# Optimization experiments

Measured on AMD Instinct MI355X. Metric: run time of the kernel, lower is better.

Reference implementation:

```python
import jax, jax.numpy as jnp
import numpy as np

TAGSET = 64
START = 0
END = 63
NEG = -10000.0


def setup_inputs() -> dict:
    key = jax.random.key(0)
    k1, k2, k3 = jax.random.split(key, 3)
    B, T, K = 256, 1024, TAGSET
    feats = jax.random.normal(k1, (B, T, K), dtype=jnp.float32)
    tags = jax.random.randint(k2, (B, T), 0, K, dtype=jnp.int64)
    masks = jnp.ones((B, T), dtype=jnp.float32)
    transitions = jax.random.normal(k3, (K, K), dtype=jnp.float32)
    transitions = transitions.at[START, :].set(NEG)
    transitions = transitions.at[:, END].set(NEG)
    return {"feats": feats, "transitions": transitions, "tags": tags, "masks": masks}


def _forward_alg(feats, transitions, masks):
    # feats: [B,T,K], masks: [B,T], transitions: [K,K]
    B, T, K = feats.shape
    alpha0 = jnp.full((B, K), NEG, dtype=feats.dtype).at[:, START].set(0.0)

    def step(alpha, xs):
        f_t, m_t = xs  # [B,K], [B]
        # transitions[i,j] + alpha[b,j], logsumexp over previous tag j
        scores = transitions[None, :, :] + alpha[:, None, :]  # [B,K,K]
        new = jax.nn.logsumexp(scores, axis=-1) + f_t  # [B,K]
        m = m_t[:, None]
        alpha = new * m + alpha * (1.0 - m)
        return alpha, None

    feats_t = jnp.swapaxes(feats[:, 1:], 0, 1)  # [T-1,B,K]
    masks_t = jnp.swapaxes(masks[:, 1:], 0, 1)  # [T-1,B]
    alpha, _ = jax.lax.scan(step, alpha0, (feats_t, masks_t))
    return jax.nn.logsumexp(alpha, axis=-1)  # [B]


def _score_sentence(feats, transitions, tags, masks):
    # transitions[tags_t, tags_{t-1}] + feats[t, tags_t], masked, summed over t>=1
    trans_score = transitions[tags[:, 1:], tags[:, :-1]]  # [B,T-1]
    emit_score = jnp.take_along_axis(feats[:, 1:], tags[:, 1:, None], axis=-1)[..., 0]
    return ((trans_score + emit_score) * masks[:, 1:]).sum(axis=-1)  # [B]


def reference(feats, transitions, tags, masks):
    forward_score = _forward_alg(feats, transitions, masks)
    gold_score = _score_sentence(feats, transitions, tags, masks)
    return jnp.mean(forward_score - gold_score)
```

## Files before the change

### kernel.cpp

```cpp
#include <hip/hip_runtime.h>

#define KK 64
#define TT 1024
#define BB 256
#define START_TAG 0

typedef float v2f __attribute__((ext_vector_type(2)));
typedef float v4f __attribute__((ext_vector_type(4)));

__device__ __forceinline__ float lane_bcast(float v, int lane) {
    return __int_as_float(__builtin_amdgcn_readlane(__float_as_int(v), lane));
}

#define PKMUL(D, S, E) asm("v_pk_mul_f32 %0, %1, %2"     : "=v"(D) : "v"(S), "v"(E));
#define PKFMA(D, S, E) asm("v_pk_fma_f32 %0, %1, %2, %0" : "+v"(D) : "v"(S), "v"(E));
#define PKADD(D, X, Y) asm("v_pk_add_f32 %0, %1, %2"     : "=v"(D) : "v"(X), "v"(Y));

#define DECLP(k) v2f et##k = { __expf(trow[2*(k)]), __expf(trow[2*(k)+1]) };
#define PINP(p,q,r,s) asm volatile("" : "+v"(et##p), "+v"(et##q), "+v"(et##r), "+v"(et##s));

#define DO_STEP(EFV, MKV, RN) { \
    abuf[i] = a; \
    const v4f* rb_ = reinterpret_cast<const v4f*>(abuf); \
    v4f w0 = rb_[0],  w1 = rb_[1],  w2 = rb_[2],  w3 = rb_[3]; \
    v4f w4 = rb_[4],  w5 = rb_[5],  w6 = rb_[6],  w7 = rb_[7]; \
    v4f w8 = rb_[8],  w9 = rb_[9],  w10 = rb_[10], w11 = rb_[11]; \
    v4f w12 = rb_[12], w13 = rb_[13], w14 = rb_[14], w15 = rb_[15]; \
    v2f acc0, acc1, acc2, acc3; \
    PKMUL(acc0, w0.xy, et0)   PKMUL(acc1, w0.zw, et1) \
    PKMUL(acc2, w1.xy, et2)   PKMUL(acc3, w1.zw, et3) \
    PKFMA(acc0, w2.xy, et4)   PKFMA(acc1, w2.zw, et5) \
    PKFMA(acc2, w3.xy, et6)   PKFMA(acc3, w3.zw, et7) \
    PKFMA(acc0, w4.xy, et8)   PKFMA(acc1, w4.zw, et9) \
    PKFMA(acc2, w5.xy, et10)  PKFMA(acc3, w5.zw, et11) \
    PKFMA(acc0, w6.xy, et12)  PKFMA(acc1, w6.zw, et13) \
    PKFMA(acc2, w7.xy, et14)  PKFMA(acc3, w7.zw, et15) \
    PKFMA(acc0, w8.xy, et16)  PKFMA(acc1, w8.zw, et17) \
    PKFMA(acc2, w9.xy, et18)  PKFMA(acc3, w9.zw, et19) \
    PKFMA(acc0, w10.xy, et20) PKFMA(acc1, w10.zw, et21) \
    PKFMA(acc2, w11.xy, et22) PKFMA(acc3, w11.zw, et23) \
    PKFMA(acc0, w12.xy, et24) PKFMA(acc1, w12.zw, et25) \
    PKFMA(acc2, w13.xy, et26) PKFMA(acc3, w13.zw, et27) \
    PKFMA(acc0, w14.xy, et28) PKFMA(acc1, w14.zw, et29) \
    PKFMA(acc2, w15.xy, et30) PKFMA(acc3, w15.zw, et31) \
    v2f accA, accB, accC; \
    PKADD(accA, acc0, acc1) \
    PKADD(accB, acc2, acc3) \
    PKADD(accC, accA, accB) \
    float s_ = accC.x + accC.y; \
    float anew = s_ * (EFV); \
    a = ((MKV) != 0.0f) ? anew : a; \
    if (RN) { \
        float a1 = fmaxf(lane_bcast(a, 1), 1e-37f); \
        a *= __builtin_amdgcn_rcpf(a1); \
        offset += __logf(a1); \
    } \
}

__global__ __launch_bounds__(64)
__attribute__((amdgpu_waves_per_eu(1, 1)))
void crf_forward_kernel(
    const float* __restrict__ feats,
    const float* __restrict__ trans,
    const float* __restrict__ masks,
    const int*   __restrict__ tags,
    float* __restrict__ out)
{
    const int b = blockIdx.x;
    const int i = threadIdx.x;

    __shared__ __align__(16) float abuf[KK];

    const float* trow = trans + i * KK;
    DECLP(0)  DECLP(1)  DECLP(2)  DECLP(3)  DECLP(4)  DECLP(5)  DECLP(6)  DECLP(7)
    DECLP(8)  DECLP(9)  DECLP(10) DECLP(11) DECLP(12) DECLP(13) DECLP(14) DECLP(15)
    DECLP(16) DECLP(17) DECLP(18) DECLP(19) DECLP(20) DECLP(21) DECLP(22) DECLP(23)
    DECLP(24) DECLP(25) DECLP(26) DECLP(27) DECLP(28) DECLP(29) DECLP(30) DECLP(31)
    PINP(0,1,2,3)     PINP(4,5,6,7)     PINP(8,9,10,11)   PINP(12,13,14,15)
    PINP(16,17,18,19) PINP(20,21,22,23) PINP(24,25,26,27) PINP(28,29,30,31)

    float a = (i == START_TAG) ? 1.0f : 0.0f;
    float offset = 0.0f;

    const float* fb = feats + (size_t)b * TT * KK;
    const float* mb = masks + (size_t)b * TT;

    float cf0 = fb[1 * KK + i], cf1 = fb[2 * KK + i];
    float cf2 = fb[3 * KK + i], cf3 = fb[4 * KK + i];
    float cm0 = mb[1], cm1 = mb[2], cm2 = mb[3], cm3 = mb[4];

    for (int t0 = 1; t0 < TT; t0 += 4) {
        int p0 = (t0 + 4 < TT) ? t0 + 4 : TT - 1;
        int p1 = (t0 + 5 < TT) ? t0 + 5 : TT - 1;
        int p2 = (t0 + 6 < TT) ? t0 + 6 : TT - 1;
        int p3 = (t0 + 7 < TT) ? t0 + 7 : TT - 1;
        float nf0 = fb[p0 * KK + i], nf1 = fb[p1 * KK + i];
        float nf2 = fb[p2 * KK + i], nf3 = fb[p3 * KK + i];
        float nm0 = mb[p0], nm1 = mb[p1], nm2 = mb[p2], nm3 = mb[p3];

        float ef0 = __expf(cf0), ef1 = __expf(cf1);
        float ef2 = __expf(cf2), ef3 = __expf(cf3);

        DO_STEP(ef0, cm0, 0)
        DO_STEP(ef1, cm1, 0)
        DO_STEP(ef2, cm2, 0)
        float m3 = (t0 + 3 < TT) ? cm3 : 0.0f;
        DO_STEP(ef3, m3, 1)

        cf0 = nf0; cf1 = nf1; cf2 = nf2; cf3 = nf3;
        cm0 = nm0; cm1 = nm1; cm2 = nm2; cm3 = nm3;
    }

    float s = a;
    #pragma unroll
    for (int off = 32; off >= 1; off >>= 1)
        s += __shfl_xor(s, off, 64);
    float fwd_score = offset + __logf(s);

    const int* tg = tags + b * TT;
    float g = 0.f;
    for (int t = 1 + i; t < TT; t += 64) {
        int ct = tg[t], pt = tg[t - 1];
        g += (trans[ct * KK + pt] + fb[t * KK + ct]) * mb[t];
    }
    #pragma unroll
    for (int off = 32; off >= 1; off >>= 1)
        g += __shfl_xor(g, off, 64);

    if (i == 0) atomicAdd(out, (fwd_score - g) * (1.0f / (float)BB));
}

extern "C" void kernel_launch(void* const* d_in, const int* in_sizes, int n_in,
                              void* d_out, int out_size, void* d_ws, size_t ws_size,
                              hipStream_t stream) {
    const float* feats = (const float*)d_in[0];
    const float* trans = (const float*)d_in[1];
    const int*   tags  = (const int*)d_in[2];
    const float* masks = (const float*)d_in[3];
    float* out = (float*)d_out;

    hipMemsetAsync(out, 0, sizeof(float), stream);
    crf_forward_kernel<<<BB, 64, 0, stream>>>(feats, trans, masks, tags, out);
}
```

Before: 297.8 us.

## Compute own-row block of alpha dot product via DPP row_ror instead of LDS

Splits each step's 64-term matrix-vector product into two parts. The 16 terms from the lane's own DPP row come from cross-lane row_ror DPP multiply/FMA on the live alpha register. The other 48 terms still come from LDS reads of the other three rows. This cuts LDS read volume per step by a quarter and overlaps DPP arithmetic with LDS latency. In exchange it adds hand-written DPP asm, s_nop hazard padding, and permuted transition exponent tables, which adds latency on the serial recurrence.

```diff
diff --git a/kernel.cpp b/kernel.cpp
--- a/kernel.cpp
+++ b/kernel.cpp
@@ -16,38 +16,49 @@
 #define PKFMA(D, S, E) asm("v_pk_fma_f32 %0, %1, %2, %0" : "+v"(D) : "v"(S), "v"(E));
 #define PKADD(D, X, Y) asm("v_pk_add_f32 %0, %1, %2"     : "=v"(D) : "v"(X), "v"(Y));
 
-#define DECLP(k) v2f et##k = { __expf(trow[2*(k)]), __expf(trow[2*(k)+1]) };
-#define PINP(p,q,r,s) asm volatile("" : "+v"(et##p), "+v"(et##q), "+v"(et##r), "+v"(et##s));
+#define RORMOVI(D, K) \
+    asm("v_mov_b32 %0, %1 row_ror:" #K " row_mask:0xf bank_mask:0xf" \
+        : "=v"(D) : "v"(lid));
+#define RORMUL(D, K, E) \
+    asm("v_mul_f32 %0, %1, %2 row_ror:" #K " row_mask:0xf bank_mask:0xf" \
+        : "=v"(D) : "v"(a), "v"(E));
+#define RORFMA(D, K, E) \
+    asm("v_fmac_f32 %0, %1, %2 row_ror:" #K " row_mask:0xf bank_mask:0xf" \
+        : "+v"(D) : "v"(a), "v"(E));
 
 #define DO_STEP(EFV, MKV, RN) { \
     abuf[i] = a; \
-    const v4f* rb_ = reinterpret_cast<const v4f*>(abuf); \
-    v4f w0 = rb_[0],  w1 = rb_[1],  w2 = rb_[2],  w3 = rb_[3]; \
-    v4f w4 = rb_[4],  w5 = rb_[5],  w6 = rb_[6],  w7 = rb_[7]; \
-    v4f w8 = rb_[8],  w9 = rb_[9],  w10 = rb_[10], w11 = rb_[11]; \
-    v4f w12 = rb_[12], w13 = rb_[13], w14 = rb_[14], w15 = rb_[15]; \
-    v2f acc0, acc1, acc2, acc3; \
-    PKMUL(acc0, w0.xy, et0)   PKMUL(acc1, w0.zw, et1) \
-    PKMUL(acc2, w1.xy, et2)   PKMUL(acc3, w1.zw, et3) \
-    PKFMA(acc0, w2.xy, et4)   PKFMA(acc1, w2.zw, et5) \
-    PKFMA(acc2, w3.xy, et6)   PKFMA(acc3, w3.zw, et7) \
-    PKFMA(acc0, w4.xy, et8)   PKFMA(acc1, w4.zw, et9) \
-    PKFMA(acc2, w5.xy, et10)  PKFMA(acc3, w5.zw, et11) \
-    PKFMA(acc0, w6.xy, et12)  PKFMA(acc1, w6.zw, et13) \
-    PKFMA(acc2, w7.xy, et14)  PKFMA(acc3, w7.zw, et15) \
-    PKFMA(acc0, w8.xy, et16)  PKFMA(acc1, w8.zw, et17) \
-    PKFMA(acc2, w9.xy, et18)  PKFMA(acc3, w9.zw, et19) \
-    PKFMA(acc0, w10.xy, et20) PKFMA(acc1, w10.zw, et21) \
-    PKFMA(acc2, w11.xy, et22) PKFMA(acc3, w11.zw, et23) \
-    PKFMA(acc0, w12.xy, et24) PKFMA(acc1, w12.zw, et25) \
-    PKFMA(acc2, w13.xy, et26) PKFMA(acc3, w13.zw, et27) \
-    PKFMA(acc0, w14.xy, et28) PKFMA(acc1, w14.zw, et29) \
-    PKFMA(acc2, w15.xy, et30) PKFMA(acc3, w15.zw, et31) \
-    v2f accA, accB, accC; \
-    PKADD(accA, acc0, acc1) \
-    PKADD(accB, acc2, acc3) \
-    PKADD(accC, accA, accB) \
-    float s_ = accC.x + accC.y; \
+    const v4f* pA_ = reinterpret_cast<const v4f*>(abuf + cb1); \
+    const v4f* pB_ = reinterpret_cast<const v4f*>(abuf + cb2); \
+    const v4f* pC_ = reinterpret_cast<const v4f*>(abuf + cb3); \
+    v4f wA0 = pA_[0], wA1 = pA_[1], wA2 = pA_[2], wA3 = pA_[3]; \
+    v4f wB0 = pB_[0], wB1 = pB_[1], wB2 = pB_[2], wB3 = pB_[3]; \
+    v4f wC0 = pC_[0], wC1 = pC_[1], wC2 = pC_[2], wC3 = pC_[3]; \
+    float sA = a * er0; \
+    float sB; RORMUL(sB, 1, er1) \
+    RORFMA(sA, 2,  er2)  RORFMA(sB, 3,  er3) \
+    RORFMA(sA, 4,  er4)  RORFMA(sB, 5,  er5) \
+    RORFMA(sA, 6,  er6)  RORFMA(sB, 7,  er7) \
+    RORFMA(sA, 8,  er8)  RORFMA(sB, 9,  er9) \
+    RORFMA(sA, 10, er10) RORFMA(sB, 11, er11) \
+    RORFMA(sA, 12, er12) RORFMA(sB, 13, er13) \
+    RORFMA(sA, 14, er14) RORFMA(sB, 15, er15) \
+    v2f q0, q1, q2, q3; \
+    PKMUL(q0, wA0.xy, eA0) PKMUL(q1, wA0.zw, eA1) \
+    PKMUL(q2, wA1.xy, eA2) PKMUL(q3, wA1.zw, eA3) \
+    PKFMA(q0, wA2.xy, eA4) PKFMA(q1, wA2.zw, eA5) \
+    PKFMA(q2, wA3.xy, eA6) PKFMA(q3, wA3.zw, eA7) \
+    PKFMA(q0, wB0.xy, eB0) PKFMA(q1, wB0.zw, eB1) \
+    PKFMA(q2, wB1.xy, eB2) PKFMA(q3, wB1.zw, eB3) \
+    PKFMA(q0, wB2.xy, eB4) PKFMA(q1, wB2.zw, eB5) \
+    PKFMA(q2, wB3.xy, eB6) PKFMA(q3, wB3.zw, eB7) \
+    PKFMA(q0, wC0.xy, eC0) PKFMA(q1, wC0.zw, eC1) \
+    PKFMA(q2, wC1.xy, eC2) PKFMA(q3, wC1.zw, eC3) \
+    PKFMA(q0, wC2.xy, eC4) PKFMA(q1, wC2.zw, eC5) \
+    PKFMA(q2, wC3.xy, eC6) PKFMA(q3, wC3.zw, eC7) \
+    v2f qA, qB, qC; \
+    PKADD(qA, q0, q1) PKADD(qB, q2, q3) PKADD(qC, qA, qB) \
+    float s_ = (qC.x + qC.y) + (sA + sB); \
     float anew = s_ * (EFV); \
     a = ((MKV) != 0.0f) ? anew : a; \
     if (RN) { \
@@ -55,7 +66,10 @@
         a *= __builtin_amdgcn_rcpf(a1); \
         offset += __logf(a1); \
     } \
+    asm volatile("s_nop 1" : "+v"(a));  \
 }
+
+#define PIN4(p,q,r,s) asm volatile("" : "+v"(p), "+v"(q), "+v"(r), "+v"(s));
 
 __global__ __launch_bounds__(64)
 __attribute__((amdgpu_waves_per_eu(1, 1)))
@@ -68,19 +82,50 @@
 {
     const int b = blockIdx.x;
     const int i = threadIdx.x;
+    const int r = (i >> 4) & 3;
+    const int rowbase = i & 48;
 
     __shared__ __align__(16) float abuf[KK];
 
     const float* trow = trans + i * KK;
-    DECLP(0)  DECLP(1)  DECLP(2)  DECLP(3)  DECLP(4)  DECLP(5)  DECLP(6)  DECLP(7)
-    DECLP(8)  DECLP(9)  DECLP(10) DECLP(11) DECLP(12) DECLP(13) DECLP(14) DECLP(15)
-    DECLP(16) DECLP(17) DECLP(18) DECLP(19) DECLP(20) DECLP(21) DECLP(22) DECLP(23)
-    DECLP(24) DECLP(25) DECLP(26) DECLP(27) DECLP(28) DECLP(29) DECLP(30) DECLP(31)
-    PINP(0,1,2,3)     PINP(4,5,6,7)     PINP(8,9,10,11)   PINP(12,13,14,15)
-    PINP(16,17,18,19) PINP(20,21,22,23) PINP(24,25,26,27) PINP(28,29,30,31)
+
+    int lid = i & 15;
+    asm volatile("s_nop 1" : "+v"(lid));
+    int x1, x2, x3, x4, x5, x6, x7, x8, x9, x10, x11, x12, x13, x14, x15;
+    RORMOVI(x1, 1)   RORMOVI(x2, 2)   RORMOVI(x3, 3)   RORMOVI(x4, 4)
+    RORMOVI(x5, 5)   RORMOVI(x6, 6)   RORMOVI(x7, 7)   RORMOVI(x8, 8)
+    RORMOVI(x9, 9)   RORMOVI(x10, 10) RORMOVI(x11, 11) RORMOVI(x12, 12)
+    RORMOVI(x13, 13) RORMOVI(x14, 14) RORMOVI(x15, 15)
+    float er0  = __expf(trow[rowbase + lid]);
+    float er1  = __expf(trow[rowbase + x1]),  er2  = __expf(trow[rowbase + x2]);
+    float er3  = __expf(trow[rowbase + x3]),  er4  = __expf(trow[rowbase + x4]);
+    float er5  = __expf(trow[rowbase + x5]),  er6  = __expf(trow[rowbase + x6]);
+    float er7  = __expf(trow[rowbase + x7]),  er8  = __expf(trow[rowbase + x8]);
+    float er9  = __expf(trow[rowbase + x9]),  er10 = __expf(trow[rowbase + x10]);
+    float er11 = __expf(trow[rowbase + x11]), er12 = __expf(trow[rowbase + x12]);
+    float er13 = __expf(trow[rowbase + x13]), er14 = __expf(trow[rowbase + x14]);
+    float er15 = __expf(trow[rowbase + x15]);
+
+    const int cb1 = ((r + 1) & 3) << 4;
+    const int cb2 = ((r + 2) & 3) << 4;
+    const int cb3 = ((r + 3) & 3) << 4;
+#define DECLE(nm, cb, p) v2f nm = { __expf(trow[(cb) + 2*(p)]), __expf(trow[(cb) + 2*(p) + 1]) };
+    DECLE(eA0, cb1, 0) DECLE(eA1, cb1, 1) DECLE(eA2, cb1, 2) DECLE(eA3, cb1, 3)
+    DECLE(eA4, cb1, 4) DECLE(eA5, cb1, 5) DECLE(eA6, cb1, 6) DECLE(eA7, cb1, 7)
+    DECLE(eB0, cb2, 0) DECLE(eB1, cb2, 1) DECLE(eB2, cb2, 2) DECLE(eB3, cb2, 3)
+    DECLE(eB4, cb2, 4) DECLE(eB5, cb2, 5) DECLE(eB6, cb2, 6) DECLE(eB7, cb2, 7)
+    DECLE(eC0, cb3, 0) DECLE(eC1, cb3, 1) DECLE(eC2, cb3, 2) DECLE(eC3, cb3, 3)
+    DECLE(eC4, cb3, 4) DECLE(eC5, cb3, 5) DECLE(eC6, cb3, 6) DECLE(eC7, cb3, 7)
+
+    PIN4(er0, er1, er2, er3)   PIN4(er4, er5, er6, er7)
+    PIN4(er8, er9, er10, er11) PIN4(er12, er13, er14, er15)
+    PIN4(eA0, eA1, eA2, eA3)   PIN4(eA4, eA5, eA6, eA7)
+    PIN4(eB0, eB1, eB2, eB3)   PIN4(eB4, eB5, eB6, eB7)
+    PIN4(eC0, eC1, eC2, eC3)   PIN4(eC4, eC5, eC6, eC7)
 
     float a = (i == START_TAG) ? 1.0f : 0.0f;
     float offset = 0.0f;
+    asm volatile("s_nop 1" : "+v"(a));
 
     const float* fb = feats + (size_t)b * TT * KK;
     const float* mb = masks + (size_t)b * TT;
```

Measured after the change: 298.4 us. About the same (+0.2%).

## Replace LDS alpha broadcast with permlane swaps and DPP row-rotate FMAs

Applied to the files above, without the earlier changes.

Each recurrence step no longer writes alpha to shared memory and reads all 64 values back. Instead, permlane32/permlane16 swaps give each lane four alpha values from different rows, and DPP row_ror FMAs sweep the 16 rotations. The exp(transition) table is re-gathered per lane to match that rotation order. This removes the LDS store-to-load latency from the serial chain, but it uses scalar FMAs instead of packed ones and depends on s_nop hazard padding for correctness.

```diff
diff --git a/kernel.cpp b/kernel.cpp
--- a/kernel.cpp
+++ b/kernel.cpp
@@ -5,49 +5,42 @@
 #define BB 256
 #define START_TAG 0
 
-typedef float v2f __attribute__((ext_vector_type(2)));
-typedef float v4f __attribute__((ext_vector_type(4)));
-
 __device__ __forceinline__ float lane_bcast(float v, int lane) {
     return __int_as_float(__builtin_amdgcn_readlane(__float_as_int(v), lane));
 }
 
-#define PKMUL(D, S, E) asm("v_pk_mul_f32 %0, %1, %2"     : "=v"(D) : "v"(S), "v"(E));
-#define PKFMA(D, S, E) asm("v_pk_fma_f32 %0, %1, %2, %0" : "+v"(D) : "v"(S), "v"(E));
-#define PKADD(D, X, Y) asm("v_pk_add_f32 %0, %1, %2"     : "=v"(D) : "v"(X), "v"(Y));
+#define SWAPL32(X, Y) asm("v_permlane32_swap_b32 %0, %1" : "+v"(X), "+v"(Y));
+#define SWAPL16(X, Y) asm("v_permlane16_swap_b32 %0, %1" : "+v"(X), "+v"(Y));
 
-#define DECLP(k) v2f et##k = { __expf(trow[2*(k)]), __expf(trow[2*(k)+1]) };
-#define PINP(p,q,r,s) asm volatile("" : "+v"(et##p), "+v"(et##q), "+v"(et##r), "+v"(et##s));
+#define RMOVI(D, S, K) \
+    asm("v_mov_b32 %0, %1 row_ror:" #K " row_mask:0xf bank_mask:0xf" \
+        : "=v"(D) : "v"(S));
+#define RFMA(D, S, K, E) \
+    asm("v_fmac_f32 %0, %1, %2 row_ror:" #K " row_mask:0xf bank_mask:0xf" \
+        : "+v"(D) : "v"(S), "v"(E));
+
+#define GATHER(dst, src, K) { int x_; RMOVI(x_, src, K) dst = __expf(trow[x_]); }
+
+#define PIN4(p,q,r,s) asm volatile("" : "+v"(p), "+v"(q), "+v"(r), "+v"(s));
+
+#define FMAROW(K) \
+    RFMA(c0, U,  K, etA##K) RFMA(c1, U2, K, etB##K) \
+    RFMA(c2, V,  K, etC##K) RFMA(c3, V2, K, etD##K)
 
 #define DO_STEP(EFV, MKV, RN) { \
-    abuf[i] = a; \
-    const v4f* rb_ = reinterpret_cast<const v4f*>(abuf); \
-    v4f w0 = rb_[0],  w1 = rb_[1],  w2 = rb_[2],  w3 = rb_[3]; \
-    v4f w4 = rb_[4],  w5 = rb_[5],  w6 = rb_[6],  w7 = rb_[7]; \
-    v4f w8 = rb_[8],  w9 = rb_[9],  w10 = rb_[10], w11 = rb_[11]; \
-    v4f w12 = rb_[12], w13 = rb_[13], w14 = rb_[14], w15 = rb_[15]; \
-    v2f acc0, acc1, acc2, acc3; \
-    PKMUL(acc0, w0.xy, et0)   PKMUL(acc1, w0.zw, et1) \
-    PKMUL(acc2, w1.xy, et2)   PKMUL(acc3, w1.zw, et3) \
-    PKFMA(acc0, w2.xy, et4)   PKFMA(acc1, w2.zw, et5) \
-    PKFMA(acc2, w3.xy, et6)   PKFMA(acc3, w3.zw, et7) \
-    PKFMA(acc0, w4.xy, et8)   PKFMA(acc1, w4.zw, et9) \
-    PKFMA(acc2, w5.xy, et10)  PKFMA(acc3, w5.zw, et11) \
-    PKFMA(acc0, w6.xy, et12)  PKFMA(acc1, w6.zw, et13) \
-    PKFMA(acc2, w7.xy, et14)  PKFMA(acc3, w7.zw, et15) \
-    PKFMA(acc0, w8.xy, et16)  PKFMA(acc1, w8.zw, et17) \
-    PKFMA(acc2, w9.xy, et18)  PKFMA(acc3, w9.zw, et19) \
-    PKFMA(acc0, w10.xy, et20) PKFMA(acc1, w10.zw, et21) \
-    PKFMA(acc2, w11.xy, et22) PKFMA(acc3, w11.zw, et23) \
-    PKFMA(acc0, w12.xy, et24) PKFMA(acc1, w12.zw, et25) \
-    PKFMA(acc2, w13.xy, et26) PKFMA(acc3, w13.zw, et27) \
-    PKFMA(acc0, w14.xy, et28) PKFMA(acc1, w14.zw, et29) \
-    PKFMA(acc2, w15.xy, et30) PKFMA(acc3, w15.zw, et31) \
-    v2f accA, accB, accC; \
-    PKADD(accA, acc0, acc1) \
-    PKADD(accB, acc2, acc3) \
-    PKADD(accC, accA, accB) \
-    float s_ = accC.x + accC.y; \
+    float U = a, V = a; \
+    asm volatile("s_nop 1" : "+v"(U), "+v"(V)); \
+    SWAPL32(U, V) \
+    float U2 = U, V2 = V; \
+    asm volatile("s_nop 1" : "+v"(U), "+v"(U2), "+v"(V), "+v"(V2)); \
+    SWAPL16(U, U2) \
+    SWAPL16(V, V2) \
+    asm volatile("s_nop 1" : "+v"(U), "+v"(U2), "+v"(V), "+v"(V2)); \
+    float c0 = U * etA0, c1 = U2 * etB0, c2 = V * etC0, c3 = V2 * etD0; \
+    FMAROW(1)  FMAROW(2)  FMAROW(3)  FMAROW(4)  FMAROW(5) \
+    FMAROW(6)  FMAROW(7)  FMAROW(8)  FMAROW(9)  FMAROW(10) \
+    FMAROW(11) FMAROW(12) FMAROW(13) FMAROW(14) FMAROW(15) \
+    float s_ = (c0 + c1) + (c2 + c3); \
     float anew = s_ * (EFV); \
     a = ((MKV) != 0.0f) ? anew : a; \
     if (RN) { \
@@ -69,15 +62,58 @@
     const int b = blockIdx.x;
     const int i = threadIdx.x;
 
-    __shared__ __align__(16) float abuf[KK];
+    const float* trow = trans + i * KK;
 
-    const float* trow = trans + i * KK;
-    DECLP(0)  DECLP(1)  DECLP(2)  DECLP(3)  DECLP(4)  DECLP(5)  DECLP(6)  DECLP(7)
-    DECLP(8)  DECLP(9)  DECLP(10) DECLP(11) DECLP(12) DECLP(13) DECLP(14) DECLP(15)
-    DECLP(16) DECLP(17) DECLP(18) DECLP(19) DECLP(20) DECLP(21) DECLP(22) DECLP(23)
-    DECLP(24) DECLP(25) DECLP(26) DECLP(27) DECLP(28) DECLP(29) DECLP(30) DECLP(31)
-    PINP(0,1,2,3)     PINP(4,5,6,7)     PINP(8,9,10,11)   PINP(12,13,14,15)
-    PINP(16,17,18,19) PINP(20,21,22,23) PINP(24,25,26,27) PINP(28,29,30,31)
+    int lid = i;
+    asm volatile("s_nop 1" : "+v"(lid));
+    int jU = lid, jV = lid;
+    asm volatile("s_nop 1" : "+v"(jU), "+v"(jV));
+    SWAPL32(jU, jV)
+    int jU2 = jU, jV2 = jV;
+    asm volatile("s_nop 1" : "+v"(jU), "+v"(jU2), "+v"(jV), "+v"(jV2));
+    SWAPL16(jU, jU2)
+    SWAPL16(jV, jV2)
+    asm volatile("s_nop 1" : "+v"(jU), "+v"(jU2), "+v"(jV), "+v"(jV2));
+
+    float etA0, etA1, etA2, etA3, etA4, etA5, etA6, etA7,
+          etA8, etA9, etA10, etA11, etA12, etA13, etA14, etA15;
+    float etB0, etB1, etB2, etB3, etB4, etB5, etB6, etB7,
+          etB8, etB9, etB10, etB11, etB12, etB13, etB14, etB15;
+    float etC0, etC1, etC2, etC3, etC4, etC5, etC6, etC7,
+          etC8, etC9, etC10, etC11, etC12, etC13, etC14, etC15;
+    float etD0, etD1, etD2, etD3, etD4, etD5, etD6, etD7,
+          etD8, etD9, etD10, etD11, etD12, etD13, etD14, etD15;
+    etA0 = __expf(trow[jU]);  etB0 = __expf(trow[jU2]);
+    etC0 = __expf(trow[jV]);  etD0 = __expf(trow[jV2]);
+    GATHER(etA1, jU, 1)   GATHER(etA2, jU, 2)   GATHER(etA3, jU, 3)
+    GATHER(etA4, jU, 4)   GATHER(etA5, jU, 5)   GATHER(etA6, jU, 6)
+    GATHER(etA7, jU, 7)   GATHER(etA8, jU, 8)   GATHER(etA9, jU, 9)
+    GATHER(etA10, jU, 10) GATHER(etA11, jU, 11) GATHER(etA12, jU, 12)
+    GATHER(etA13, jU, 13) GATHER(etA14, jU, 14) GATHER(etA15, jU, 15)
+    GATHER(etB1, jU2, 1)   GATHER(etB2, jU2, 2)   GATHER(etB3, jU2, 3)
+    GATHER(etB4, jU2, 4)   GATHER(etB5, jU2, 5)   GATHER(etB6, jU2, 6)
+    GATHER(etB7, jU2, 7)   GATHER(etB8, jU2, 8)   GATHER(etB9, jU2, 9)
+    GATHER(etB10, jU2, 10) GATHER(etB11, jU2, 11) GATHER(etB12, jU2, 12)
+    GATHER(etB13, jU2, 13) GATHER(etB14, jU2, 14) GATHER(etB15, jU2, 15)
+    GATHER(etC1, jV, 1)   GATHER(etC2, jV, 2)   GATHER(etC3, jV, 3)
+    GATHER(etC4, jV, 4)   GATHER(etC5, jV, 5)   GATHER(etC6, jV, 6)
+    GATHER(etC7, jV, 7)   GATHER(etC8, jV, 8)   GATHER(etC9, jV, 9)
+    GATHER(etC10, jV, 10) GATHER(etC11, jV, 11) GATHER(etC12, jV, 12)
+    GATHER(etC13, jV, 13) GATHER(etC14, jV, 14) GATHER(etC15, jV, 15)
+    GATHER(etD1, jV2, 1)   GATHER(etD2, jV2, 2)   GATHER(etD3, jV2, 3)
+    GATHER(etD4, jV2, 4)   GATHER(etD5, jV2, 5)   GATHER(etD6, jV2, 6)
+    GATHER(etD7, jV2, 7)   GATHER(etD8, jV2, 8)   GATHER(etD9, jV2, 9)
+    GATHER(etD10, jV2, 10) GATHER(etD11, jV2, 11) GATHER(etD12, jV2, 12)
+    GATHER(etD13, jV2, 13) GATHER(etD14, jV2, 14) GATHER(etD15, jV2, 15)
+
+    PIN4(etA0, etA1, etA2, etA3)     PIN4(etA4, etA5, etA6, etA7)
+    PIN4(etA8, etA9, etA10, etA11)   PIN4(etA12, etA13, etA14, etA15)
+    PIN4(etB0, etB1, etB2, etB3)     PIN4(etB4, etB5, etB6, etB7)
+    PIN4(etB8, etB9, etB10, etB11)   PIN4(etB12, etB13, etB14, etB15)
+    PIN4(etC0, etC1, etC2, etC3)     PIN4(etC4, etC5, etC6, etC7)
+    PIN4(etC8, etC9, etC10, etC11)   PIN4(etC12, etC13, etC14, etC15)
+    PIN4(etD0, etD1, etD2, etD3)     PIN4(etD4, etD5, etD6, etD7)
+    PIN4(etD8, etD9, etD10, etD11)   PIN4(etD12, etD13, etD14, etD15)
 
     float a = (i == START_TAG) ? 1.0f : 0.0f;
     float offset = 0.0f;
```

Result: slower. 338.8 us (+13.8%).
